# Optimization experiments

Measured on AMD Instinct MI355X. Metric: run time of the kernel, lower is better.

Reference implementation:

```python
import jax, jax.numpy as jnp
import numpy as np

N_HEADS = 16
D_MODEL = 2048
DK = D_MODEL // N_HEADS
SEQ = 2048


def setup_inputs() -> dict:
    key = jax.random.key(0)
    ks = jax.random.split(key, 11)
    s = 0.02
    return {
        "query": jax.random.normal(ks[0], (SEQ, D_MODEL), jnp.float32),
        "key": jax.random.normal(ks[1], (SEQ, D_MODEL), jnp.float32),
        "value": jax.random.normal(ks[2], (SEQ, D_MODEL), jnp.float32),
        # per-head projection weights, stacked over heads: [H, d_model, dk]
        "Wq": jax.random.normal(ks[3], (N_HEADS, D_MODEL, DK), jnp.float32) * s,
        "bq": jnp.zeros((N_HEADS, DK), jnp.float32),
        "Wk": jax.random.normal(ks[4], (N_HEADS, D_MODEL, DK), jnp.float32) * s,
        "bk": jnp.zeros((N_HEADS, DK), jnp.float32),
        "Wv": jax.random.normal(ks[5], (N_HEADS, D_MODEL, DK), jnp.float32) * s,
        "bv": jnp.zeros((N_HEADS, DK), jnp.float32),
        # output projection: [H*dk, d_model]
        "Wo": jax.random.normal(ks[6], (N_HEADS * DK, D_MODEL), jnp.float32) * s,
        "bo": jnp.zeros((D_MODEL,), jnp.float32),
    }


def reference(query, key, value, Wq, bq, Wk, bk, Wv, bv, Wo, bo):
    # Per-head linear projections, batched over heads. q/k/v: [H, S, dk]
    q = jnp.einsum('sd,hdk->hsk', query, Wq) + bq[:, None, :]
    k = jnp.einsum('sd,hdk->hsk', key, Wk) + bk[:, None, :]
    v = jnp.einsum('sd,hdk->hsk', value, Wv) + bv[:, None, :]
    scale = jnp.sqrt(jnp.asarray(DK, q.dtype))
    # scores: [H, S_q, S_k]
    scores = jnp.einsum('hsk,htk->hst', q, k) / scale
    # Faithful to original: Softmax(dim=0) on each 2D [S_q, S_k] matrix
    # -> normalize over the QUERY axis (axis=1 here).
    attn = jax.nn.softmax(scores, axis=1)
    heads = jnp.einsum('hst,htk->hsk', attn, v)  # [H, S, dk]
    # torch.cat(attentions, dim=1): [S, H*dk]
    concat = jnp.transpose(heads, (1, 0, 2)).reshape(SEQ, N_HEADS * DK)
    return concat @ Wo + bo
```

## Files before the change

kernel.cpp:

```cpp
#include <hip/hip_runtime.h>

#define SEQ 2048
#define DMODEL 2048
#define NHEADS 16
#define DKH 128

typedef __bf16 bf16;
typedef __attribute__((ext_vector_type(8))) __bf16 bf16x8;
typedef __attribute__((ext_vector_type(4))) __bf16 bf16x4;
typedef __attribute__((ext_vector_type(4))) float f32x4;

#define AS1 __attribute__((address_space(1)))
#define AS3 __attribute__((address_space(3)))

__device__ __forceinline__ void async_copy16(const void* g, void* l) {
  __builtin_amdgcn_global_load_lds((AS1 void*)(unsigned long long)g,
                                   (AS3 void*)l, 16, 0, 0);
}

__device__ __forceinline__ int swz(int chunk, int row) {
  return (chunk ^ (row & 7)) << 3;
}
__device__ __forceinline__ int swz16(int chunk, int row) {
  return (chunk ^ (row & 15)) << 3;
}

template <typename OutT, bool BIAS>
__global__ __launch_bounds__(256) void gemm_bt(
    const bf16* __restrict__ A, const bf16* __restrict__ B,
    const float* __restrict__ bias, OutT* __restrict__ C,
    int M, int N, int K, int lda, int ldb, int ldo, float scale,
    long long sA, long long sB, long long sC, long long sBias) {
  A += (long long)blockIdx.z * sA;
  B += (long long)blockIdx.z * sB;
  C += (long long)blockIdx.z * sC;
  const float* biasp = BIAS ? (bias + (long long)blockIdx.z * sBias) : nullptr;

  const int m0 = blockIdx.y * 128;
  const int n0 = blockIdx.x * 128;

  __shared__ __align__(16) bf16 As[128 * 64];
  __shared__ __align__(16) bf16 Bs[128 * 64];

  const int tid = threadIdx.x;
  const int wave = tid >> 6;
  const int lane = tid & 63;
  const int srow = wave * 8 + (lane >> 3);
  const int scol = ((lane & 7) ^ (lane >> 3)) * 8;
  const int wr = (wave >> 1) * 64;
  const int wc = (wave & 1) * 64;
  const int lr = lane & 15;
  const int quad = lane >> 4;

  const bf16* ag = A + (long long)(m0 + srow) * lda + scol;
  const bf16* bg = B + (long long)(n0 + srow) * ldb + scol;

  f32x4 acc[4][4];
#pragma unroll
  for (int i = 0; i < 4; ++i)
#pragma unroll
    for (int j = 0; j < 4; ++j) {
      acc[i][j][0] = 0.f; acc[i][j][1] = 0.f;
      acc[i][j][2] = 0.f; acc[i][j][3] = 0.f;
    }

  for (int kt = 0; kt < K; kt += 64) {
#pragma unroll
    for (int i = 0; i < 4; ++i) {
      async_copy16(ag + kt + (long long)i * 32 * lda, As + (i * 32 + wave * 8) * 64);
      async_copy16(bg + kt + (long long)i * 32 * ldb, Bs + (i * 32 + wave * 8) * 64);
    }
    __syncthreads();
#pragma unroll
    for (int kk = 0; kk < 64; kk += 32) {
      bf16x8 af[4], bfr[4];
#pragma unroll
      for (int i = 0; i < 4; ++i) {
        const int ra = wr + i * 16 + lr;
        const int rb = wc + i * 16 + lr;
        af[i]  = *(const bf16x8*)(As + ra * 64 + swz((kk >> 3) + quad, ra));
        bfr[i] = *(const bf16x8*)(Bs + rb * 64 + swz((kk >> 3) + quad, rb));
      }
#pragma unroll
      for (int i = 0; i < 4; ++i)
#pragma unroll
        for (int j = 0; j < 4; ++j)
          acc[i][j] = __builtin_amdgcn_mfma_f32_16x16x32_bf16(af[i], bfr[j], acc[i][j], 0, 0, 0);
    }
    __syncthreads();
  }

#pragma unroll
  for (int j = 0; j < 4; ++j) {
    const int n = n0 + wc + j * 16 + lr;
    const float bv = BIAS ? biasp[n] : 0.f;
#pragma unroll
    for (int i = 0; i < 4; ++i) {
      const int mb = m0 + wr + i * 16 + quad * 4;
#pragma unroll
      for (int r = 0; r < 4; ++r)
        C[(long long)(mb + r) * ldo + n] = (OutT)(acc[i][j][r] * scale + bv);
    }
  }
}

__global__ __launch_bounds__(256) void qk_exp(
    const bf16* __restrict__ q, const bf16* __restrict__ k,
    bf16* __restrict__ E, float* __restrict__ lpart) {
  const int h = blockIdx.z;
  const int m0 = blockIdx.y * 128;
  const int nstrip = blockIdx.x * 512;
  const bf16* A = q + (long long)h * DKH;
  const bf16* B = k + (long long)h * DKH;
  bf16* C = E + (long long)h * SEQ * SEQ;

  __shared__ __align__(16) bf16 As[128 * 128];
  __shared__ __align__(16) bf16 Bs[128 * 128];

  const int tid = threadIdx.x;
  const int wave = tid >> 6;
  const int lane = tid & 63;
  const int wr = (wave >> 1) * 64;
  const int wc = (wave & 1) * 64;
  const int lr = lane & 15;
  const int quad = lane >> 4;
  const float scale = 0.08838834764831845f;

  for (int nt = 0; nt < 4; ++nt) {
    if (nt) __syncthreads();
#pragma unroll
    for (int it = 0; it < 8; ++it) {
      const int row = wave * 32 + it * 4 + (lane >> 4);
      const int chunk = (lane & 15) ^ (row & 15);
      async_copy16(B + (long long)(nstrip + nt * 128 + row) * DMODEL + chunk * 8,
                   Bs + (wave * 32 + it * 4) * 128);
    }
    if (nt == 0) {
#pragma unroll
      for (int it = 0; it < 8; ++it) {
        const int row = wave * 32 + it * 4 + (lane >> 4);
        const int chunk = (lane & 15) ^ (row & 15);
        async_copy16(A + (long long)(m0 + row) * DMODEL + chunk * 8,
                     As + (wave * 32 + it * 4) * 128);
      }
    }
    __syncthreads();

    f32x4 acc[4][4];
#pragma unroll
    for (int i = 0; i < 4; ++i)
#pragma unroll
      for (int j = 0; j < 4; ++j) {
        acc[i][j][0] = 0.f; acc[i][j][1] = 0.f;
        acc[i][j][2] = 0.f; acc[i][j][3] = 0.f;
      }

#pragma unroll
    for (int kk = 0; kk < 128; kk += 32) {
      bf16x8 af[4], bfr[4];
#pragma unroll
      for (int i = 0; i < 4; ++i) {
        const int ra = wr + i * 16 + lr;
        const int rb = wc + i * 16 + lr;
        af[i]  = *(const bf16x8*)(As + ra * 128 + swz16((kk >> 3) + quad, ra));
        bfr[i] = *(const bf16x8*)(Bs + rb * 128 + swz16((kk >> 3) + quad, rb));
      }
#pragma unroll
      for (int i = 0; i < 4; ++i)
#pragma unroll
        for (int j = 0; j < 4; ++j)
          acc[i][j] = __builtin_amdgcn_mfma_f32_16x16x32_bf16(af[i], bfr[j], acc[i][j], 0, 0, 0);
    }

#pragma unroll
    for (int j = 0; j < 4; ++j) {
      const int n = nstrip + nt * 128 + wc + j * 16 + lr;
      float l_loc = 0.f;
#pragma unroll
      for (int i = 0; i < 4; ++i) {
        const int mb = m0 + wr + i * 16 + quad * 4;
#pragma unroll
        for (int r = 0; r < 4; ++r) {
          bf16 ev = (bf16)__expf(acc[i][j][r] * scale);
          C[(long long)(mb + r) * SEQ + n] = ev;
          l_loc += (float)ev;
        }
      }
      l_loc += __shfl_xor(l_loc, 16, 64);
      l_loc += __shfl_xor(l_loc, 32, 64);
      if (quad == 0)
        lpart[((long long)h * 32 + blockIdx.y * 2 + (wave >> 1)) * SEQ + n] = l_loc;
    }
  }
}

__global__ void sm_sum(const float* __restrict__ lp, float* __restrict__ rvec) {
  const int i = blockIdx.x * 256 + threadIdx.x;
  const int h = i >> 11, t = i & (SEQ - 1);
  float l = 0.f;
#pragma unroll
  for (int rb = 0; rb < 32; ++rb)
    l += lp[((long long)h * 32 + rb) * SEQ + t];
  rvec[i] = 1.f / l;
}

__global__ void vscale(bf16* __restrict__ vt, const float* __restrict__ rvec) {
  const int cg = blockIdx.y;
  const int t0 = threadIdx.x * 8;
  const float* r = rvec + (cg >> 7) * SEQ;
  bf16x8 v = *(const bf16x8*)(vt + (long long)cg * SEQ + t0);
#pragma unroll
  for (int e = 0; e < 8; ++e) v[e] = (bf16)((float)v[e] * r[t0 + e]);
  *(bf16x8*)(vt + (long long)cg * SEQ + t0) = v;
}

__global__ __launch_bounds__(256) void pv_gemm(
    const bf16* __restrict__ Sc, const bf16* __restrict__ VT,
    bf16* __restrict__ O) {
  const int h = blockIdx.y;
  const int m0 = blockIdx.x * 64;
  const bf16* A = Sc + (long long)h * SEQ * SEQ;
  const bf16* B = VT + (long long)h * DKH * SEQ;

  __shared__ __align__(16) bf16 As[64 * 64];
  __shared__ __align__(16) bf16 Bs[128 * 64];

  const int tid = threadIdx.x;
  const int wave = tid >> 6;
  const int lane = tid & 63;
  const int srow = wave * 8 + (lane >> 3);
  const int scol = ((lane & 7) ^ (lane >> 3)) * 8;
  const int wr = (wave >> 1) * 32;
  const int wc = (wave & 1) * 64;
  const int lr = lane & 15;
  const int quad = lane >> 4;

  const bf16* ag = A + (long long)(m0 + srow) * SEQ + scol;
  const bf16* bg = B + (long long)srow * SEQ + scol;

  f32x4 acc[2][4];
#pragma unroll
  for (int i = 0; i < 2; ++i)
#pragma unroll
    for (int j = 0; j < 4; ++j) {
      acc[i][j][0] = 0.f; acc[i][j][1] = 0.f;
      acc[i][j][2] = 0.f; acc[i][j][3] = 0.f;
    }

  for (int kt = 0; kt < SEQ; kt += 64) {
#pragma unroll
    for (int i = 0; i < 2; ++i)
      async_copy16(ag + kt + (long long)i * 32 * SEQ, As + (i * 32 + wave * 8) * 64);
#pragma unroll
    for (int i = 0; i < 4; ++i)
      async_copy16(bg + kt + (long long)i * 32 * SEQ, Bs + (i * 32 + wave * 8) * 64);
    __syncthreads();
#pragma unroll
    for (int kk = 0; kk < 64; kk += 32) {
      bf16x8 af[2], bfr[4];
#pragma unroll
      for (int i = 0; i < 2; ++i) {
        const int ra = wr + i * 16 + lr;
        af[i] = *(const bf16x8*)(As + ra * 64 + swz((kk >> 3) + quad, ra));
      }
#pragma unroll
      for (int j = 0; j < 4; ++j) {
        const int rb = wc + j * 16 + lr;
        bfr[j] = *(const bf16x8*)(Bs + rb * 64 + swz((kk >> 3) + quad, rb));
      }
#pragma unroll
      for (int i = 0; i < 2; ++i)
#pragma unroll
        for (int j = 0; j < 4; ++j)
          acc[i][j] = __builtin_amdgcn_mfma_f32_16x16x32_bf16(af[i], bfr[j], acc[i][j], 0, 0, 0);
    }
    __syncthreads();
  }

#pragma unroll
  for (int j = 0; j < 4; ++j) {
    const int c = h * DKH + wc + j * 16 + lr;
#pragma unroll
    for (int i = 0; i < 2; ++i) {
      const int mb = m0 + wr + i * 16 + quad * 4;
#pragma unroll
      for (int r = 0; r < 4; ++r)
        O[(long long)(mb + r) * DMODEL + c] = (bf16)acc[i][j][r];
    }
  }
}

__global__ void reduce_bias(const float* __restrict__ p, const float* __restrict__ bo,
                            float* __restrict__ out) {
  const long long i = ((long long)blockIdx.x * 256 + threadIdx.x) * 4;
  const float4 a = *(const float4*)(p + i);
  const float4 b = *(const float4*)(p + (long long)SEQ * DMODEL + i);
  const float4 bb = *(const float4*)(bo + (i & (DMODEL - 1)));
  float4 o;
  o.x = a.x + b.x + bb.x; o.y = a.y + b.y + bb.y;
  o.z = a.z + b.z + bb.z; o.w = a.w + b.w + bb.w;
  *(float4*)(out + i) = o;
}

__global__ void cvt3_f32_to_bf16(const float* __restrict__ a, const float* __restrict__ b,
                                 const float* __restrict__ c, bf16* __restrict__ out,
                                 long long n) {
  const float* src = blockIdx.z == 0 ? a : (blockIdx.z == 1 ? b : c);
  long long i = ((long long)blockIdx.x * blockDim.x + threadIdx.x) * 4;
  if (i >= n) return;
  const float4 v = *(const float4*)(src + i);
  bf16x4 o;
  o[0] = (bf16)v.x; o[1] = (bf16)v.y; o[2] = (bf16)v.z; o[3] = (bf16)v.w;
  *(bf16x4*)(out + blockIdx.z * n + i) = o;
}

__global__ void transposeW3(const float* __restrict__ Wq, const float* __restrict__ Wk,
                            const float* __restrict__ Wv, bf16* __restrict__ out) {
  __shared__ float tile[32][33];
  const int z = blockIdx.z;
  const int g = z >> 4, hh = z & 15;
  const float* in = (g == 0 ? Wq : (g == 1 ? Wk : Wv)) + (long long)hh * DMODEL * DKH;
  bf16* o = out + (long long)z * DMODEL * DKH;
  const int c0 = blockIdx.x * 32, r0 = blockIdx.y * 32;
  const int tx = threadIdx.x, ty = threadIdx.y;
#pragma unroll
  for (int j = 0; j < 32; j += 8)
    tile[ty + j][tx] = in[(long long)(r0 + ty + j) * DKH + c0 + tx];
  __syncthreads();
#pragma unroll
  for (int j = 0; j < 32; j += 8)
    o[(long long)(c0 + ty + j) * DMODEL + r0 + tx] = (bf16)tile[tx][ty + j];
}

template <typename T>
__global__ void transpose_to_bf16(const T* __restrict__ in, bf16* __restrict__ out,
                                  int R, int Cc) {
  __shared__ float tile[32][33];
  const int c0 = blockIdx.x * 32, r0 = blockIdx.y * 32;
  const int tx = threadIdx.x, ty = threadIdx.y;
#pragma unroll
  for (int j = 0; j < 32; j += 8)
    tile[ty + j][tx] = (float)in[(long long)(r0 + ty + j) * Cc + c0 + tx];
  __syncthreads();
#pragma unroll
  for (int j = 0; j < 32; j += 8)
    out[(long long)(c0 + ty + j) * R + r0 + tx] = (bf16)tile[tx][ty + j];
}

__global__ void pack_bias3(const float* __restrict__ a, const float* __restrict__ b,
                           const float* __restrict__ c, float* __restrict__ o) {
  int i = blockIdx.x * 256 + threadIdx.x;
  if (i < NHEADS * DKH) {
    o[i] = a[i];
    o[NHEADS * DKH + i] = b[i];
    o[2 * NHEADS * DKH + i] = c[i];
  }
}

extern "C" void kernel_launch(void* const* d_in, const int* in_sizes, int n_in,
                              void* d_out, int out_size, void* d_ws, size_t ws_size,
                              hipStream_t stream) {
  const float* query = (const float*)d_in[0];
  const float* key_  = (const float*)d_in[1];
  const float* value = (const float*)d_in[2];
  const float* Wq = (const float*)d_in[3];
  const float* bq = (const float*)d_in[4];
  const float* Wk = (const float*)d_in[5];
  const float* bk = (const float*)d_in[6];
  const float* Wv = (const float*)d_in[7];
  const float* bv = (const float*)d_in[8];
  const float* Wo = (const float*)d_in[9];
  const float* bo = (const float*)d_in[10];
  float* out = (float*)d_out;

  const long long elems = (long long)SEQ * DMODEL;
  const long long SZB = elems * 2;

  char* ws = (char*)d_ws;
  bf16* Qb = (bf16*)ws;
  bf16* Wt = (bf16*)(ws + 3 * SZB);
  bf16* scores = (bf16*)ws;
  float* Opart = (float*)ws;
  char* p = ws + (long long)NHEADS * SEQ * SEQ * 2;
  float* biasQKV = (float*)p; p += 32 * 1024;
  bf16* Wot   = (bf16*)p; p += SZB;
  bf16* qkv   = (bf16*)p; p += 3 * SZB;
  bf16* vt    = (bf16*)p; p += SZB;
  bf16* heads = (bf16*)p; p += SZB;
  float* lpart = (float*)p; p += (long long)NHEADS * 32 * SEQ * 4;
  float* rvec  = (float*)p; p += (long long)NHEADS * SEQ * 4;
  if ((size_t)(p - ws) > ws_size) return;

  cvt3_f32_to_bf16<<<dim3(elems / 1024, 1, 3), 256, 0, stream>>>(query, key_, value, Qb, elems);
  transposeW3<<<dim3(DKH / 32, DMODEL / 32, 48), dim3(32, 8), 0, stream>>>(Wq, Wk, Wv, Wt);
  transpose_to_bf16<float><<<dim3(DMODEL / 32, DMODEL / 32), dim3(32, 8), 0, stream>>>(Wo, Wot, DMODEL, DMODEL);
  pack_bias3<<<(NHEADS * DKH + 255) / 256, 256, 0, stream>>>(bq, bk, bv, biasQKV);

  gemm_bt<bf16, true><<<dim3(16, 16, 3), 256, 0, stream>>>(
      Qb, Wt, biasQKV, qkv, SEQ, DMODEL, DMODEL, DMODEL, DMODEL, DMODEL, 1.f,
      elems, elems, elems, (long long)DMODEL);

  transpose_to_bf16<bf16><<<dim3(DMODEL / 32, SEQ / 32), dim3(32, 8), 0, stream>>>(
      qkv + 2 * elems, vt, SEQ, DMODEL);

  qk_exp<<<dim3(4, 16, NHEADS), 256, 0, stream>>>(qkv, qkv + elems, scores, lpart);

  sm_sum<<<NHEADS * SEQ / 256, 256, 0, stream>>>(lpart, rvec);

  vscale<<<dim3(1, DMODEL), 256, 0, stream>>>(vt, rvec);

  pv_gemm<<<dim3(SEQ / 64, NHEADS), 256, 0, stream>>>(scores, vt, heads);

  gemm_bt<float, false><<<dim3(16, 16, 2), 256, 0, stream>>>(
      heads, Wot, nullptr, Opart, SEQ, DMODEL, 1024, DMODEL, DMODEL, DMODEL, 1.f,
      1024, 1024, elems, 0);

  reduce_bias<<<elems / 1024, 256, 0, stream>>>(Opart, bo, out);
}
```

Baseline: 353.2 us.

## Fuse prep kernels, write V transposed from QKV GEMM, shrink qk_exp tiles

Four preprocessing kernels (input conversion, weight transposes, bias packing) are merged into one launch that dispatches on block index. The QKV projection GEMM now writes the V slice straight into transposed layout, which drops the separate V transpose kernel. qk_exp switches to 64-column B tiles over 8 iterations and loads the Q tile once before the loop, which cuts its shared memory and accumulator registers and should raise occupancy. The transposed V stores are 8-byte scattered writes with a stride of SEQ, so they may coalesce poorly.

```diff
diff --git a/kernel.cpp b/kernel.cpp
--- a/kernel.cpp
+++ b/kernel.cpp
@@ -30,7 +30,8 @@
     const bf16* __restrict__ A, const bf16* __restrict__ B,
     const float* __restrict__ bias, OutT* __restrict__ C,
     int M, int N, int K, int lda, int ldb, int ldo, float scale,
-    long long sA, long long sB, long long sC, long long sBias) {
+    long long sA, long long sB, long long sC, long long sBias,
+    bf16* __restrict__ CT) {
   A += (long long)blockIdx.z * sA;
   B += (long long)blockIdx.z * sB;
   C += (long long)blockIdx.z * sC;
@@ -90,6 +91,23 @@
     __syncthreads();
   }
 
+  if (BIAS && CT != nullptr && blockIdx.z == 2) {
+#pragma unroll
+    for (int j = 0; j < 4; ++j) {
+      const int n = n0 + wc + j * 16 + lr;
+      const float bv = biasp[n];
+#pragma unroll
+      for (int i = 0; i < 4; ++i) {
+        const int mb = m0 + wr + i * 16 + quad * 4;
+        bf16x4 o;
+#pragma unroll
+        for (int r = 0; r < 4; ++r) o[r] = (bf16)(acc[i][j][r] * scale + bv);
+        *(bf16x4*)(CT + (long long)n * SEQ + mb) = o;
+      }
+    }
+    return;
+  }
+
 #pragma unroll
   for (int j = 0; j < 4; ++j) {
     const int n = n0 + wc + j * 16 + lr;
@@ -115,66 +133,68 @@
   bf16* C = E + (long long)h * SEQ * SEQ;
 
   __shared__ __align__(16) bf16 As[128 * 128];
-  __shared__ __align__(16) bf16 Bs[128 * 128];
+  __shared__ __align__(16) bf16 Bs[64 * 128];
 
   const int tid = threadIdx.x;
   const int wave = tid >> 6;
   const int lane = tid & 63;
   const int wr = (wave >> 1) * 64;
-  const int wc = (wave & 1) * 64;
+  const int wc = (wave & 1) * 32;
   const int lr = lane & 15;
   const int quad = lane >> 4;
   const float scale = 0.08838834764831845f;
 
-  for (int nt = 0; nt < 4; ++nt) {
+#pragma unroll
+  for (int it = 0; it < 8; ++it) {
+    const int row = wave * 32 + it * 4 + (lane >> 4);
+    const int chunk = (lane & 15) ^ (row & 15);
+    async_copy16(A + (long long)(m0 + row) * DMODEL + chunk * 8,
+                 As + (wave * 32 + it * 4) * 128);
+  }
+
+  for (int nt = 0; nt < 8; ++nt) {
     if (nt) __syncthreads();
 #pragma unroll
-    for (int it = 0; it < 8; ++it) {
-      const int row = wave * 32 + it * 4 + (lane >> 4);
+    for (int it = 0; it < 4; ++it) {
+      const int row = wave * 16 + it * 4 + (lane >> 4);
       const int chunk = (lane & 15) ^ (row & 15);
-      async_copy16(B + (long long)(nstrip + nt * 128 + row) * DMODEL + chunk * 8,
-                   Bs + (wave * 32 + it * 4) * 128);
-    }
-    if (nt == 0) {
-#pragma unroll
-      for (int it = 0; it < 8; ++it) {
-        const int row = wave * 32 + it * 4 + (lane >> 4);
-        const int chunk = (lane & 15) ^ (row & 15);
-        async_copy16(A + (long long)(m0 + row) * DMODEL + chunk * 8,
-                     As + (wave * 32 + it * 4) * 128);
-      }
-    }
-    __syncthreads();
-
-    f32x4 acc[4][4];
+      async_copy16(B + (long long)(nstrip + nt * 64 + row) * DMODEL + chunk * 8,
+                   Bs + (wave * 16 + it * 4) * 128);
+    }
+    __syncthreads();
+
+    f32x4 acc[4][2];
 #pragma unroll
     for (int i = 0; i < 4; ++i)
 #pragma unroll
-      for (int j = 0; j < 4; ++j) {
+      for (int j = 0; j < 2; ++j) {
         acc[i][j][0] = 0.f; acc[i][j][1] = 0.f;
         acc[i][j][2] = 0.f; acc[i][j][3] = 0.f;
       }
 
 #pragma unroll
     for (int kk = 0; kk < 128; kk += 32) {
-      bf16x8 af[4], bfr[4];
+      bf16x8 af[4], bfr[2];
 #pragma unroll
       for (int i = 0; i < 4; ++i) {
         const int ra = wr + i * 16 + lr;
-        const int rb = wc + i * 16 + lr;
-        af[i]  = *(const bf16x8*)(As + ra * 128 + swz16((kk >> 3) + quad, ra));
-        bfr[i] = *(const bf16x8*)(Bs + rb * 128 + swz16((kk >> 3) + quad, rb));
+        af[i] = *(const bf16x8*)(As + ra * 128 + swz16((kk >> 3) + quad, ra));
+      }
+#pragma unroll
+      for (int j = 0; j < 2; ++j) {
+        const int rb = wc + j * 16 + lr;
+        bfr[j] = *(const bf16x8*)(Bs + rb * 128 + swz16((kk >> 3) + quad, rb));
       }
 #pragma unroll
       for (int i = 0; i < 4; ++i)
 #pragma unroll
-        for (int j = 0; j < 4; ++j)
+        for (int j = 0; j < 2; ++j)
           acc[i][j] = __builtin_amdgcn_mfma_f32_16x16x32_bf16(af[i], bfr[j], acc[i][j], 0, 0, 0);
     }
 
 #pragma unroll
-    for (int j = 0; j < 4; ++j) {
-      const int n = nstrip + nt * 128 + wc + j * 16 + lr;
+    for (int j = 0; j < 2; ++j) {
+      const int n = nstrip + nt * 64 + wc + j * 16 + lr;
       float l_loc = 0.f;
 #pragma unroll
       for (int i = 0; i < 4; ++i) {
@@ -302,58 +322,70 @@
   *(float4*)(out + i) = o;
 }
 
-__global__ void cvt3_f32_to_bf16(const float* __restrict__ a, const float* __restrict__ b,
-                                 const float* __restrict__ c, bf16* __restrict__ out,
-                                 long long n) {
-  const float* src = blockIdx.z == 0 ? a : (blockIdx.z == 1 ? b : c);
-  long long i = ((long long)blockIdx.x * blockDim.x + threadIdx.x) * 4;
-  if (i >= n) return;
-  const float4 v = *(const float4*)(src + i);
-  bf16x4 o;
-  o[0] = (bf16)v.x; o[1] = (bf16)v.y; o[2] = (bf16)v.z; o[3] = (bf16)v.w;
-  *(bf16x4*)(out + blockIdx.z * n + i) = o;
-}
-
-__global__ void transposeW3(const float* __restrict__ Wq, const float* __restrict__ Wk,
-                            const float* __restrict__ Wv, bf16* __restrict__ out) {
+__global__ __launch_bounds__(256) void prep(
+    const float* __restrict__ q, const float* __restrict__ k,
+    const float* __restrict__ v,
+    const float* __restrict__ Wq, const float* __restrict__ Wk,
+    const float* __restrict__ Wv, const float* __restrict__ Wo,
+    const float* __restrict__ bq, const float* __restrict__ bk,
+    const float* __restrict__ bv,
+    bf16* __restrict__ Qb, bf16* __restrict__ Wt, bf16* __restrict__ Wot,
+    float* __restrict__ biasQKV) {
   __shared__ float tile[32][33];
-  const int z = blockIdx.z;
-  const int g = z >> 4, hh = z & 15;
-  const float* in = (g == 0 ? Wq : (g == 1 ? Wk : Wv)) + (long long)hh * DMODEL * DKH;
-  bf16* o = out + (long long)z * DMODEL * DKH;
-  const int c0 = blockIdx.x * 32, r0 = blockIdx.y * 32;
-  const int tx = threadIdx.x, ty = threadIdx.y;
-#pragma unroll
-  for (int j = 0; j < 32; j += 8)
-    tile[ty + j][tx] = in[(long long)(r0 + ty + j) * DKH + c0 + tx];
-  __syncthreads();
-#pragma unroll
-  for (int j = 0; j < 32; j += 8)
-    o[(long long)(c0 + ty + j) * DMODEL + r0 + tx] = (bf16)tile[tx][ty + j];
-}
-
-template <typename T>
-__global__ void transpose_to_bf16(const T* __restrict__ in, bf16* __restrict__ out,
-                                  int R, int Cc) {
-  __shared__ float tile[32][33];
-  const int c0 = blockIdx.x * 32, r0 = blockIdx.y * 32;
-  const int tx = threadIdx.x, ty = threadIdx.y;
-#pragma unroll
-  for (int j = 0; j < 32; j += 8)
-    tile[ty + j][tx] = (float)in[(long long)(r0 + ty + j) * Cc + c0 + tx];
-  __syncthreads();
-#pragma unroll
-  for (int j = 0; j < 32; j += 8)
-    out[(long long)(c0 + ty + j) * R + r0 + tx] = (bf16)tile[tx][ty + j];
-}
-
-__global__ void pack_bias3(const float* __restrict__ a, const float* __restrict__ b,
-                           const float* __restrict__ c, float* __restrict__ o) {
-  int i = blockIdx.x * 256 + threadIdx.x;
-  if (i < NHEADS * DKH) {
-    o[i] = a[i];
-    o[NHEADS * DKH + i] = b[i];
-    o[2 * NHEADS * DKH + i] = c[i];
+  const long long elems = (long long)SEQ * DMODEL;
+  const int id = blockIdx.x;
+  const int tid = threadIdx.x;
+
+  if (id < 12288) {
+    const float* src = (id < 4096) ? q : (id < 8192) ? k : v;
+    const int t = id >> 12;
+    const long long i = (long long)(id & 4095) * 1024 + tid * 4;
+    const float4 vv = *(const float4*)(src + i);
+    bf16x4 o;
+    o[0] = (bf16)vv.x; o[1] = (bf16)vv.y; o[2] = (bf16)vv.z; o[3] = (bf16)vv.w;
+    *(bf16x4*)(Qb + (long long)t * elems + i) = o;
+    return;
+  }
+  const int tx = tid & 31, ty = tid >> 5;
+  if (id < 24576) {
+    const int rel = id - 12288;
+    const int z = rel >> 8;
+    const int inner = rel & 255;
+    const int bx = inner & 3;
+    const int by = inner >> 2;
+    const int g = z >> 4, hh = z & 15;
+    const float* in = (g == 0 ? Wq : (g == 1 ? Wk : Wv)) + (long long)hh * DMODEL * DKH;
+    bf16* o = Wt + (long long)z * DMODEL * DKH;
+    const int c0 = bx * 32, r0 = by * 32;
+#pragma unroll
+    for (int j = 0; j < 32; j += 8)
+      tile[ty + j][tx] = in[(long long)(r0 + ty + j) * DKH + c0 + tx];
+    __syncthreads();
+#pragma unroll
+    for (int j = 0; j < 32; j += 8)
+      o[(long long)(c0 + ty + j) * DMODEL + r0 + tx] = (bf16)tile[tx][ty + j];
+    return;
+  }
+  if (id < 28672) {
+    const int rel = id - 24576;
+    const int bx = rel & 63, by = rel >> 6;
+    const int c0 = bx * 32, r0 = by * 32;
+#pragma unroll
+    for (int j = 0; j < 32; j += 8)
+      tile[ty + j][tx] = Wo[(long long)(r0 + ty + j) * DMODEL + c0 + tx];
+    __syncthreads();
+#pragma unroll
+    for (int j = 0; j < 32; j += 8)
+      Wot[(long long)(c0 + ty + j) * DMODEL + r0 + tx] = (bf16)tile[tx][ty + j];
+    return;
+  }
+  {
+    const int i = (id - 28672) * 256 + tid;
+    if (i < NHEADS * DKH) {
+      biasQKV[i] = bq[i];
+      biasQKV[NHEADS * DKH + i] = bk[i];
+      biasQKV[2 * NHEADS * DKH + i] = bv[i];
+    }
   }
 }
 
@@ -391,17 +423,12 @@
   float* rvec  = (float*)p; p += (long long)NHEADS * SEQ * 4;
   if ((size_t)(p - ws) > ws_size) return;
 
-  cvt3_f32_to_bf16<<<dim3(elems / 1024, 1, 3), 256, 0, stream>>>(query, key_, value, Qb, elems);
-  transposeW3<<<dim3(DKH / 32, DMODEL / 32, 48), dim3(32, 8), 0, stream>>>(Wq, Wk, Wv, Wt);
-  transpose_to_bf16<float><<<dim3(DMODEL / 32, DMODEL / 32), dim3(32, 8), 0, stream>>>(Wo, Wot, DMODEL, DMODEL);
-  pack_bias3<<<(NHEADS * DKH + 255) / 256, 256, 0, stream>>>(bq, bk, bv, biasQKV);
+  prep<<<28680, 256, 0, stream>>>(query, key_, value, Wq, Wk, Wv, Wo,
+                                  bq, bk, bv, Qb, Wt, Wot, biasQKV);
 
   gemm_bt<bf16, true><<<dim3(16, 16, 3), 256, 0, stream>>>(
       Qb, Wt, biasQKV, qkv, SEQ, DMODEL, DMODEL, DMODEL, DMODEL, DMODEL, 1.f,
-      elems, elems, elems, (long long)DMODEL);
-
-  transpose_to_bf16<bf16><<<dim3(DMODEL / 32, SEQ / 32), dim3(32, 8), 0, stream>>>(
-      qkv + 2 * elems, vt, SEQ, DMODEL);
+      elems, elems, elems, (long long)DMODEL, vt);
 
   qk_exp<<<dim3(4, 16, NHEADS), 256, 0, stream>>>(qkv, qkv + elems, scores, lpart);
 
@@ -413,7 +440,7 @@
 
   gemm_bt<float, false><<<dim3(16, 16, 2), 256, 0, stream>>>(
       heads, Wot, nullptr, Opart, SEQ, DMODEL, 1024, DMODEL, DMODEL, DMODEL, 1.f,
-      1024, 1024, elems, 0);
+      1024, 1024, elems, 0, nullptr);
 
   reduce_bias<<<elems / 1024, 256, 0, stream>>>(Opart, bo, out);
 }
```

Measured after the change: 365.0 us. 1.03x slower.
